# Kernel optimization log

Hardware: AMD Instinct MI355X
Metric: run time of the kernel (lower is better)

Reference implementation:

```python
import jax, jax.numpy as jnp
import numpy as np

EMBED_DIM = 512
NUM_HEADS = 8
HEAD_DIM = EMBED_DIM // NUM_HEADS


def setup_inputs() -> dict:
    key = jax.random.key(0)
    ks = jax.random.split(key, 6)
    B, S, E = 2, 4096, EMBED_DIM
    scale = 1.0 / np.sqrt(E)
    return {
        "rotation_params": jax.random.normal(ks[0], (E, E), jnp.float32) * scale,
        "entangle_params": jax.random.normal(ks[1], (E, E), jnp.float32) * scale,
        "inputs": jax.random.normal(ks[2], (B, S, E), jnp.float32),
        "w_q": jax.random.normal(ks[3], (E, E), jnp.float32) * scale,
        "w_k": jax.random.normal(ks[4], (E, E), jnp.float32) * scale,
        "w_v": jax.random.normal(ks[5], (E, E), jnp.float32) * scale,
    }


def reference(rotation_params, entangle_params, inputs, w_q, w_k, w_v):
    B, S, E = inputs.shape
    H, D = NUM_HEADS, HEAD_DIM
    # torch nn.Linear(x) = x @ W.T ; then extra matmul with rotation/entangle mats
    q = (inputs @ w_q.T) @ rotation_params  # [B,S,E]
    k = (inputs @ w_k.T) @ entangle_params  # [B,S,E]
    v = inputs @ w_v.T                       # [B,S,E]
    # split heads -> [B,H,S,D]
    q = q.reshape(B, S, H, D).transpose(0, 2, 1, 3)
    k = k.reshape(B, S, H, D).transpose(0, 2, 1, 3)
    v = v.reshape(B, S, H, D).transpose(0, 2, 1, 3)
    scores = jnp.einsum("bhqd,bhkd->bhqk", q, k) / jnp.sqrt(jnp.float32(D))
    attn = jax.nn.softmax(scores, axis=-1)  # dropout p=0 (eval) -> identity
    out = jnp.einsum("bhqk,bhkd->bhqd", attn, v)
    return out.transpose(0, 2, 1, 3).reshape(B, S, E)
```

## Files before the change

kernel.cpp:

```cpp
#include <hip/hip_runtime.h>
#include <cstddef>

#define E 512
#define H 8
#define D 64
#define BATCH 2
#define SEQ 4096

typedef __attribute__((ext_vector_type(8))) short bf16x8;
typedef __attribute__((ext_vector_type(4))) float f32x4;
typedef __attribute__((ext_vector_type(16))) float f32x16;
typedef __attribute__((ext_vector_type(4))) unsigned uint4v;

__device__ __forceinline__ ushort f2bf(float f) {
  unsigned u = __builtin_bit_cast(unsigned, f);
  u += 0x7fff + ((u >> 16) & 1);
  return (ushort)(u >> 16);
}
__device__ __forceinline__ float bf2f(ushort h) {
  return __builtin_bit_cast(float, (unsigned)h << 16);
}
__device__ __forceinline__ unsigned pk_bf16(float lo, float hi) {
#if __has_builtin(__builtin_amdgcn_cvt_pk_bf16_f32)
  typedef __attribute__((ext_vector_type(2))) __bf16 bfv2;
  bfv2 r = __builtin_amdgcn_cvt_pk_bf16_f32(lo, hi);
  return __builtin_bit_cast(unsigned, r);
#else
  return (unsigned)f2bf(lo) | ((unsigned)f2bf(hi) << 16);
#endif
}
__device__ __forceinline__ float fexp2(float x) {
#if __has_builtin(__builtin_amdgcn_exp2f)
  return __builtin_amdgcn_exp2f(x);
#else
  return exp2f(x);
#endif
}
__device__ __forceinline__ void permswap32(unsigned& a, unsigned& b) {
  asm("v_permlane32_swap_b32 %0, %1" : "+v"(a), "+v"(b));
}

__device__ __forceinline__ void cvt8_hl(float4 a, float4 b, uint4& hw,
                                        uint4& lw) {
  float v0 = a.x, v1 = a.y, v2 = a.z, v3 = a.w;
  float v4 = b.x, v5 = b.y, v6 = b.z, v7 = b.w;
  ushort h0 = f2bf(v0), h1 = f2bf(v1), h2 = f2bf(v2), h3 = f2bf(v3);
  ushort h4 = f2bf(v4), h5 = f2bf(v5), h6 = f2bf(v6), h7 = f2bf(v7);
  hw.x = (unsigned)h0 | ((unsigned)h1 << 16);
  hw.y = (unsigned)h2 | ((unsigned)h3 << 16);
  hw.z = (unsigned)h4 | ((unsigned)h5 << 16);
  hw.w = (unsigned)h6 | ((unsigned)h7 << 16);
  lw.x = (unsigned)f2bf(v0 - bf2f(h0)) | ((unsigned)f2bf(v1 - bf2f(h1)) << 16);
  lw.y = (unsigned)f2bf(v2 - bf2f(h2)) | ((unsigned)f2bf(v3 - bf2f(h3)) << 16);
  lw.z = (unsigned)f2bf(v4 - bf2f(h4)) | ((unsigned)f2bf(v5 - bf2f(h5)) << 16);
  lw.w = (unsigned)f2bf(v6 - bf2f(h6)) | ((unsigned)f2bf(v7 - bf2f(h7)) << 16);
}

__global__ __launch_bounds__(256) void fold_tiled(
    const float* __restrict__ wq, const float* __restrict__ wk,
    const float* __restrict__ rot, const float* __restrict__ ent,
    const float* __restrict__ wv, ushort* __restrict__ weffbT) {
  const int z = blockIdx.z;
  const int k = blockIdx.x * 256 + threadIdx.x;
  const int n0 = blockIdx.y * 4;
  if (z == 2) {
#pragma unroll
    for (int t = 0; t < 4; ++t)
      weffbT[(size_t)2 * E * E + (size_t)(n0 + t) * E + k] =
          f2bf(wv[(size_t)(n0 + t) * E + k]);
    return;
  }
  const float* w = z ? wk : wq;
  const float* r = z ? ent : rot;
  float acc[4] = {};
  for (int j0 = 0; j0 < E; j0 += 16) {
    float wv_[16];
#pragma unroll
    for (int u = 0; u < 16; ++u) wv_[u] = w[(size_t)(j0 + u) * E + k];
#pragma unroll
    for (int u = 0; u < 16; ++u)
#pragma unroll
      for (int t = 0; t < 4; ++t)
        acc[t] += wv_[u] * r[(size_t)(j0 + u) * E + n0 + t];
  }
#pragma unroll
  for (int t = 0; t < 4; ++t)
    weffbT[(size_t)z * E * E + (size_t)(n0 + t) * E + k] = f2bf(acc[t]);
}

#define LDQ 72
#define LDS_S 136

__global__ __launch_bounds__(512, 4) void qkv_fused(
    const float* __restrict__ xg, const ushort* __restrict__ weffbT,
    ushort* __restrict__ qg, ushort* __restrict__ kg,
    ushort* __restrict__ vtg) {
  __shared__ ushort sm[(128 + 128 + 192) * LDQ];
  ushort* Ah = sm;
  ushort* Al = sm + 128 * LDQ;
  ushort* Bs = sm + 256 * LDQ;
  ushort* vt_lds = Bs;

  const int lin = blockIdx.y * 8 + blockIdx.x;
  const int nl = (lin & 7) * 64 + (lin >> 3);
  const int head = nl & 7;
  const int m0 = (nl >> 3) * 128;

  const int tid = threadIdx.x;
  const int wave = tid >> 6, lane = tid & 63;
  const int l31 = lane & 31, hi = lane >> 5;
  const int wm = wave & 3, wn = wave >> 2;

  const int ar = tid >> 2, ac8 = (tid & 3) * 8;
  const int b1r = tid >> 2;
  const int b2r = 128 + ((tid >> 2) & 63);

  const float* xrow = xg + (size_t)(m0 + ar) * E + ac8;
  const ushort* b1row =
      weffbT + (size_t)(b1r >> 6) * E * E + (size_t)(head * 64 + (b1r & 63)) * E + ac8;
  const ushort* b2row =
      weffbT + (size_t)2 * E * E + (size_t)(head * 64 + (b2r & 63)) * E + ac8;

  f32x16 acc[3];
  acc[0] = 0.f;
  acc[1] = 0.f;
  acc[2] = 0.f;

  const ushort* Ar = Ah + (wm * 32 + l31) * LDQ;
  const ushort* Lr = Al + (wm * 32 + l31) * LDQ;
  const ushort* Br = Bs + (wn * 96 + l31) * LDQ;

  float4 xv0 = *(const float4*)&xrow[0];
  float4 xv1 = *(const float4*)&xrow[4];
  uint4 pb1 = *(const uint4*)&b1row[0];
  uint4 pb2 = (tid < 256) ? *(const uint4*)&b2row[0] : uint4{0, 0, 0, 0};

  for (int k0 = 0; k0 < E; k0 += 32) {
    __syncthreads();
    {
      uint4 hw, lw;
      cvt8_hl(xv0, xv1, hw, lw);
      *(uint4*)&Ah[ar * LDQ + ac8] = hw;
      *(uint4*)&Al[ar * LDQ + ac8] = lw;
    }
    *(uint4*)&Bs[b1r * LDQ + ac8] = pb1;
    if (tid < 256) *(uint4*)&Bs[b2r * LDQ + ac8] = pb2;
    __syncthreads();

    const int kn = (k0 + 32 < E) ? k0 + 32 : 0;
    xv0 = *(const float4*)&xrow[kn];
    xv1 = *(const float4*)&xrow[kn + 4];
    pb1 = *(const uint4*)&b1row[kn];
    if (tid < 256) pb2 = *(const uint4*)&b2row[kn];

#pragma unroll
    for (int ks = 0; ks < 2; ++ks) {
      bf16x8 ah = *(const bf16x8*)&Ar[ks * 16 + hi * 8];
      bf16x8 al = *(const bf16x8*)&Lr[ks * 16 + hi * 8];
#pragma unroll
      for (int t = 0; t < 3; ++t) {
        bf16x8 bf = *(const bf16x8*)&Br[t * 32 * LDQ + ks * 16 + hi * 8];
        acc[t] =
            __builtin_amdgcn_mfma_f32_32x32x16_bf16(ah, bf, acc[t], 0, 0, 0);
        acc[t] =
            __builtin_amdgcn_mfma_f32_32x32x16_bf16(al, bf, acc[t], 0, 0, 0);
      }
    }
  }

  const int b = m0 >> 12;
  const int s_base = m0 & (SEQ - 1);
  const float QSCALE = 0.125f * 1.44269504f;

#pragma unroll
  for (int t = 0; t < 3; ++t) {
    const int n0 = wn * 96 + t * 32;
    const int w = n0 >> 6;
    if (w != 2) {
      ushort* dst = (w == 0) ? qg : kg;
      const float sc = (w == 0) ? QSCALE : 1.0f;
      const int d = (n0 & 63) + l31;
#pragma unroll
      for (int r = 0; r < 16; ++r) {
        float v = acc[t][r] * sc;
        float vo = __shfl_xor(v, 1);
        if (!(lane & 1)) {
          int s = s_base + wm * 32 + (r & 3) + 8 * (r >> 2) + 4 * hi;
          size_t ix = ((size_t)(b * H + head) * SEQ + s) * D + d;
          *(unsigned*)&dst[ix] = pk_bf16(v, vo);
        }
      }
    }
  }

  __syncthreads();
  if (wn == 1) {
#pragma unroll
    for (int t = 1; t < 3; ++t) {
      const int d = (t - 1) * 32 + l31;
#pragma unroll
      for (int g = 0; g < 4; ++g) {
        uint2 w2;
        w2.x = pk_bf16(acc[t][g * 4 + 0], acc[t][g * 4 + 1]);
        w2.y = pk_bf16(acc[t][g * 4 + 2], acc[t][g * 4 + 3]);
        int s = wm * 32 + 8 * g + 4 * hi;
        *(uint2*)&vt_lds[d * LDS_S + s] = w2;
      }
    }
  }
  __syncthreads();
  {
    int vr = tid >> 3, vs = (tid & 7) * 16;
    uint4 c0 = *(const uint4*)&vt_lds[vr * LDS_S + vs];
    uint4 c1 = *(const uint4*)&vt_lds[vr * LDS_S + vs + 8];
    size_t vo = ((size_t)(b * H + head) * D + vr) * SEQ + s_base + vs;
    *(uint4*)&vtg[vo] = c0;
    *(uint4*)&vtg[vo + 8] = c1;
  }
}

#define LDK 72

__global__ __launch_bounds__(512, 4) void attn_mfma(
    const ushort* __restrict__ qg, const ushort* __restrict__ kg,
    const ushort* __restrict__ vtg, float* __restrict__ out) {
  __shared__ ushort sm[4 * 64 * LDK + 256];
  ushort* Ks0 = sm;
  ushort* Vs0 = sm + 2 * 64 * LDK;
  float* lex = (float*)(sm + 4 * 64 * LDK);

  const int qt = blockIdx.x;
  const int bh = blockIdx.y;
  const int tid = threadIdx.x;
  const int wave = tid >> 6;
  const int grp = wave >> 2, wq = wave & 3;
  const int lane = tid & 63;
  const int l31 = lane & 31, hi = lane >> 5;
  const int gtid = tid & 255;

  const ushort* qp = qg + (size_t)bh * SEQ * D;
  const ushort* kp = kg + (size_t)bh * SEQ * D;
  const ushort* vp = vtg + (size_t)bh * D * SEQ;
  ushort* Ksg = Ks0 + grp * 64 * LDK;
  ushort* Vsg = Vs0 + grp * 64 * LDK;

  const int qrow0 = qt * 128 + wq * 32;
  bf16x8 qf[4];
#pragma unroll
  for (int ds = 0; ds < 4; ++ds)
    qf[ds] =
        *(const bf16x8*)&qp[(size_t)(qrow0 + l31) * D + ds * 16 + hi * 8];

  f32x16 o[2];
  o[0] = 0.f;
  o[1] = 0.f;
  float l_r = 0.f;

  const int r0 = gtid >> 3, c0 = (gtid & 7) * 8;
  const int r1 = 32 + r0;

  uint4 pk0 = *(const uint4*)&kp[(size_t)(grp * 64 + r0) * D + c0];
  uint4 pk1 = *(const uint4*)&kp[(size_t)(grp * 64 + r1) * D + c0];
  uint4 pv0 = *(const uint4*)&vp[(size_t)r0 * SEQ + grp * 64 + c0];
  uint4 pv1 = *(const uint4*)&vp[(size_t)r1 * SEQ + grp * 64 + c0];

  for (int it = 0; it < SEQ / 128; ++it) {
    __syncthreads();
    *(uint4*)&Ksg[r0 * LDK + c0] = pk0;
    *(uint4*)&Ksg[r1 * LDK + c0] = pk1;
    *(uint4*)&Vsg[r0 * LDK + c0] = pv0;
    *(uint4*)&Vsg[r1 * LDK + c0] = pv1;
    __syncthreads();

    {
      const int itn = (it + 1 < SEQ / 128) ? it + 1 : it;
      const int ktn = itn * 2 + grp;
      const ushort* ksrc = kp + (size_t)ktn * 64 * D;
      pk0 = *(const uint4*)&ksrc[r0 * D + c0];
      pk1 = *(const uint4*)&ksrc[r1 * D + c0];
      pv0 = *(const uint4*)&vp[(size_t)r0 * SEQ + ktn * 64 + c0];
      pv1 = *(const uint4*)&vp[(size_t)r1 * SEQ + ktn * 64 + c0];
    }

    __builtin_amdgcn_s_setprio(1);
    f32x16 st0 = 0.f, st1 = 0.f;
#pragma unroll
    for (int ds = 0; ds < 4; ++ds) {
      bf16x8 kf0 = *(const bf16x8*)&Ksg[(l31)*LDK + ds * 16 + hi * 8];
      bf16x8 kf1 = *(const bf16x8*)&Ksg[(32 + l31) * LDK + ds * 16 + hi * 8];
      st0 = __builtin_amdgcn_mfma_f32_32x32x16_bf16(kf0, qf[ds], st0, 0, 0, 0);
      st1 = __builtin_amdgcn_mfma_f32_32x32x16_bf16(kf1, qf[ds], st1, 0, 0, 0);
    }

    bf16x8 pf00, pf01;
    {
      float pv[16];
#pragma unroll
      for (int r = 0; r < 16; ++r) pv[r] = fexp2(st0[r]);
      float s01 = (pv[0] + pv[1]) + (pv[2] + pv[3]);
      float s23 = (pv[4] + pv[5]) + (pv[6] + pv[7]);
      float s45 = (pv[8] + pv[9]) + (pv[10] + pv[11]);
      float s67 = (pv[12] + pv[13]) + (pv[14] + pv[15]);
      l_r += (s01 + s23) + (s45 + s67);
      unsigned w0[4], w1[4];
#pragma unroll
      for (int j = 0; j < 2; ++j) {
        {
          unsigned c0w = pk_bf16(pv[2 * j + 0], pv[2 * j + 1]);
          unsigned c1w = pk_bf16(pv[2 * j + 4], pv[2 * j + 5]);
          permswap32(c0w, c1w);
          w0[j] = c0w;
          w0[2 + j] = c1w;
        }
        {
          unsigned c0w = pk_bf16(pv[2 * j + 8], pv[2 * j + 9]);
          unsigned c1w = pk_bf16(pv[2 * j + 12], pv[2 * j + 13]);
          permswap32(c0w, c1w);
          w1[j] = c0w;
          w1[2 + j] = c1w;
        }
      }
      pf00 = __builtin_bit_cast(bf16x8, (uint4v){w0[0], w0[1], w0[2], w0[3]});
      pf01 = __builtin_bit_cast(bf16x8, (uint4v){w1[0], w1[1], w1[2], w1[3]});
    }
#pragma unroll
    for (int nt = 0; nt < 2; ++nt) {
      bf16x8 vf0 = *(const bf16x8*)&Vsg[(nt * 32 + l31) * LDK + hi * 8];
      o[nt] =
          __builtin_amdgcn_mfma_f32_32x32x16_bf16(pf00, vf0, o[nt], 0, 0, 0);
      bf16x8 vf1 = *(const bf16x8*)&Vsg[(nt * 32 + l31) * LDK + 16 + hi * 8];
      o[nt] =
          __builtin_amdgcn_mfma_f32_32x32x16_bf16(pf01, vf1, o[nt], 0, 0, 0);
    }

    bf16x8 pf10, pf11;
    {
      float pv[16];
#pragma unroll
      for (int r = 0; r < 16; ++r) pv[r] = fexp2(st1[r]);
      float s01 = (pv[0] + pv[1]) + (pv[2] + pv[3]);
      float s23 = (pv[4] + pv[5]) + (pv[6] + pv[7]);
      float s45 = (pv[8] + pv[9]) + (pv[10] + pv[11]);
      float s67 = (pv[12] + pv[13]) + (pv[14] + pv[15]);
      l_r += (s01 + s23) + (s45 + s67);
      unsigned w0[4], w1[4];
#pragma unroll
      for (int j = 0; j < 2; ++j) {
        {
          unsigned c0w = pk_bf16(pv[2 * j + 0], pv[2 * j + 1]);
          unsigned c1w = pk_bf16(pv[2 * j + 4], pv[2 * j + 5]);
          permswap32(c0w, c1w);
          w0[j] = c0w;
          w0[2 + j] = c1w;
        }
        {
          unsigned c0w = pk_bf16(pv[2 * j + 8], pv[2 * j + 9]);
          unsigned c1w = pk_bf16(pv[2 * j + 12], pv[2 * j + 13]);
          permswap32(c0w, c1w);
          w1[j] = c0w;
          w1[2 + j] = c1w;
        }
      }
      pf10 = __builtin_bit_cast(bf16x8, (uint4v){w0[0], w0[1], w0[2], w0[3]});
      pf11 = __builtin_bit_cast(bf16x8, (uint4v){w1[0], w1[1], w1[2], w1[3]});
    }
#pragma unroll
    for (int nt = 0; nt < 2; ++nt) {
      bf16x8 vf0 = *(const bf16x8*)&Vsg[(nt * 32 + l31) * LDK + 32 + hi * 8];
      o[nt] =
          __builtin_amdgcn_mfma_f32_32x32x16_bf16(pf10, vf0, o[nt], 0, 0, 0);
      bf16x8 vf1 = *(const bf16x8*)&Vsg[(nt * 32 + l31) * LDK + 48 + hi * 8];
      o[nt] =
          __builtin_amdgcn_mfma_f32_32x32x16_bf16(pf11, vf1, o[nt], 0, 0, 0);
    }
    __builtin_amdgcn_s_setprio(0);
  }

  __syncthreads();
  float lg = l_r + __shfl_xor(l_r, 32);
  float* Oex = (float*)sm;
  if (grp == 1) {
#pragma unroll
    for (int nt = 0; nt < 2; ++nt)
#pragma unroll
      for (int r = 0; r < 16; ++r) {
        int row = (r & 3) + 8 * (r >> 2) + 4 * hi;
        Oex[(wq * 32 + row) * 68 + nt * 32 + l31] = o[nt][r];
      }
    if (lane < 32) lex[wq * 32 + l31] = lg;
  }
  __syncthreads();
  if (grp == 0) {
    float linv = 1.f / (lg + lex[wq * 32 + l31]);
    const int b = bh >> 3, h = bh & 7;
#pragma unroll
    for (int r = 0; r < 16; ++r) {
      int row = (r & 3) + 8 * (r >> 2) + 4 * hi;
      float inv = __shfl(linv, row);
      int srow = qt * 128 + wq * 32 + row;
#pragma unroll
      for (int nt = 0; nt < 2; ++nt) {
        float val = o[nt][r] + Oex[(wq * 32 + row) * 68 + nt * 32 + l31];
        out[((size_t)b * SEQ + srow) * E + h * D + nt * 32 + l31] = val * inv;
      }
    }
  }
}

extern "C" void kernel_launch(void* const* d_in, const int* in_sizes, int n_in,
                              void* d_out, int out_size, void* d_ws,
                              size_t ws_size, hipStream_t stream) {
  const float* rot = (const float*)d_in[0];
  const float* ent = (const float*)d_in[1];
  const float* x = (const float*)d_in[2];
  const float* wq = (const float*)d_in[3];
  const float* wk = (const float*)d_in[4];
  const float* wv = (const float*)d_in[5];
  float* out = (float*)d_out;

  const size_t NX = (size_t)BATCH * SEQ * E;
  ushort* weffbT = (ushort*)d_ws;
  ushort* qg = weffbT + 3 * E * E;
  ushort* kg = qg + NX;
  ushort* vtg = kg + NX;

  fold_tiled<<<dim3(E / 256, E / 4, 3), 256, 0, stream>>>(wq, wk, rot, ent, wv,
                                                          weffbT);
  qkv_fused<<<dim3(H, BATCH * SEQ / 128), 512, 0, stream>>>(x, weffbT, qg, kg,
                                                            vtg);
  attn_mfma<<<dim3(SEQ / 128, BATCH * H), 512, 0, stream>>>(qg, kg, vtg, out);
}
```

Baseline: 226.4 us.

## Split attention key range across four wave groups with 64-row query tiles

The attention kernel now gives each block 64 query rows handled by 2 waves per group, and splits every 128-key chunk across 4 groups of 32 keys instead of 2 groups of 64. The grid doubles and launch bounds request 8 blocks per CU, for more parallelism and better latency hiding. A shared 128-key K/V tile is loaded cooperatively each iteration. The cost is a two-stage cross-group reduction of partial outputs and denominators through LDS with extra barriers, and K/V reloads per block double because each block covers fewer query rows.

```diff
diff --git a/kernel.cpp b/kernel.cpp
--- a/kernel.cpp
+++ b/kernel.cpp
@@ -220,31 +220,28 @@
 }
 
 #define LDK 72
-
-__global__ __launch_bounds__(512, 4) void attn_mfma(
+#define LDV 136
+
+__global__ __launch_bounds__(512, 8) void attn_mfma(
     const ushort* __restrict__ qg, const ushort* __restrict__ kg,
     const ushort* __restrict__ vtg, float* __restrict__ out) {
-  __shared__ ushort sm[4 * 64 * LDK + 256];
-  ushort* Ks0 = sm;
-  ushort* Vs0 = sm + 2 * 64 * LDK;
-  float* lex = (float*)(sm + 4 * 64 * LDK);
+  __shared__ ushort Kall[128 * LDK];
+  __shared__ ushort Vall[64 * LDV];
+  __shared__ float lexA[64], lexB[64];
 
   const int qt = blockIdx.x;
   const int bh = blockIdx.y;
   const int tid = threadIdx.x;
   const int wave = tid >> 6;
-  const int grp = wave >> 2, wq = wave & 3;
+  const int grp = wave >> 1, wq = wave & 1;
   const int lane = tid & 63;
   const int l31 = lane & 31, hi = lane >> 5;
-  const int gtid = tid & 255;
 
   const ushort* qp = qg + (size_t)bh * SEQ * D;
   const ushort* kp = kg + (size_t)bh * SEQ * D;
   const ushort* vp = vtg + (size_t)bh * D * SEQ;
-  ushort* Ksg = Ks0 + grp * 64 * LDK;
-  ushort* Vsg = Vs0 + grp * 64 * LDK;
-
-  const int qrow0 = qt * 128 + wq * 32;
+
+  const int qrow0 = qt * 64 + wq * 32;
   bf16x8 qf[4];
 #pragma unroll
   for (int ds = 0; ds < 4; ++ds)
@@ -256,47 +253,48 @@
   o[1] = 0.f;
   float l_r = 0.f;
 
-  const int r0 = gtid >> 3, c0 = (gtid & 7) * 8;
-  const int r1 = 32 + r0;
-
-  uint4 pk0 = *(const uint4*)&kp[(size_t)(grp * 64 + r0) * D + c0];
-  uint4 pk1 = *(const uint4*)&kp[(size_t)(grp * 64 + r1) * D + c0];
-  uint4 pv0 = *(const uint4*)&vp[(size_t)r0 * SEQ + grp * 64 + c0];
-  uint4 pv1 = *(const uint4*)&vp[(size_t)r1 * SEQ + grp * 64 + c0];
+  const int kr = tid >> 2, kc = (tid & 3) * 16;
+  const int vr = tid >> 3, vc = (tid & 7) * 16;
+
+  uint4 pk0 = *(const uint4*)&kp[(size_t)kr * D + kc];
+  uint4 pk1 = *(const uint4*)&kp[(size_t)kr * D + kc + 8];
+  uint4 pv0 = *(const uint4*)&vp[(size_t)vr * SEQ + vc];
+  uint4 pv1 = *(const uint4*)&vp[(size_t)vr * SEQ + vc + 8];
+
+  const int kb = grp * 32;
 
   for (int it = 0; it < SEQ / 128; ++it) {
     __syncthreads();
-    *(uint4*)&Ksg[r0 * LDK + c0] = pk0;
-    *(uint4*)&Ksg[r1 * LDK + c0] = pk1;
-    *(uint4*)&Vsg[r0 * LDK + c0] = pv0;
-    *(uint4*)&Vsg[r1 * LDK + c0] = pv1;
+    *(uint4*)&Kall[kr * LDK + kc] = pk0;
+    *(uint4*)&Kall[kr * LDK + kc + 8] = pk1;
+    *(uint4*)&Vall[vr * LDV + vc] = pv0;
+    *(uint4*)&Vall[vr * LDV + vc + 8] = pv1;
     __syncthreads();
 
     {
       const int itn = (it + 1 < SEQ / 128) ? it + 1 : it;
-      const int ktn = itn * 2 + grp;
-      const ushort* ksrc = kp + (size_t)ktn * 64 * D;
-      pk0 = *(const uint4*)&ksrc[r0 * D + c0];
-      pk1 = *(const uint4*)&ksrc[r1 * D + c0];
-      pv0 = *(const uint4*)&vp[(size_t)r0 * SEQ + ktn * 64 + c0];
-      pv1 = *(const uint4*)&vp[(size_t)r1 * SEQ + ktn * 64 + c0];
+      const int base = itn * 128;
+      pk0 = *(const uint4*)&kp[(size_t)(base + kr) * D + kc];
+      pk1 = *(const uint4*)&kp[(size_t)(base + kr) * D + kc + 8];
+      pv0 = *(const uint4*)&vp[(size_t)vr * SEQ + base + vc];
+      pv1 = *(const uint4*)&vp[(size_t)vr * SEQ + base + vc + 8];
     }
 
     __builtin_amdgcn_s_setprio(1);
-    f32x16 st0 = 0.f, st1 = 0.f;
+    f32x16 st = 0.f;
 #pragma unroll
     for (int ds = 0; ds < 4; ++ds) {
-      bf16x8 kf0 = *(const bf16x8*)&Ksg[(l31)*LDK + ds * 16 + hi * 8];
-      bf16x8 kf1 = *(const bf16x8*)&Ksg[(32 + l31) * LDK + ds * 16 + hi * 8];
-      st0 = __builtin_amdgcn_mfma_f32_32x32x16_bf16(kf0, qf[ds], st0, 0, 0, 0);
-      st1 = __builtin_amdgcn_mfma_f32_32x32x16_bf16(kf1, qf[ds], st1, 0, 0, 0);
-    }
-
-    bf16x8 pf00, pf01;
+      bf16x8 kf =
+          *(const bf16x8*)&Kall[(kb + l31) * LDK + ds * 16 + hi * 8];
+      st = __builtin_amdgcn_mfma_f32_32x32x16_bf16(kf, qf[ds], st, 0, 0, 0);
+    }
+    __builtin_amdgcn_s_setprio(0);
+
+    bf16x8 pf0, pf1;
     {
       float pv[16];
 #pragma unroll
-      for (int r = 0; r < 16; ++r) pv[r] = fexp2(st0[r]);
+      for (int r = 0; r < 16; ++r) pv[r] = fexp2(st[r]);
       float s01 = (pv[0] + pv[1]) + (pv[2] + pv[3]);
       float s23 = (pv[4] + pv[5]) + (pv[6] + pv[7]);
       float s45 = (pv[8] + pv[9]) + (pv[10] + pv[11]);
@@ -320,87 +318,92 @@
           w1[2 + j] = c1w;
         }
       }
-      pf00 = __builtin_bit_cast(bf16x8, (uint4v){w0[0], w0[1], w0[2], w0[3]});
-      pf01 = __builtin_bit_cast(bf16x8, (uint4v){w1[0], w1[1], w1[2], w1[3]});
-    }
+      pf0 = __builtin_bit_cast(bf16x8, (uint4v){w0[0], w0[1], w0[2], w0[3]});
+      pf1 = __builtin_bit_cast(bf16x8, (uint4v){w1[0], w1[1], w1[2], w1[3]});
+    }
+
+    __builtin_amdgcn_s_setprio(1);
 #pragma unroll
     for (int nt = 0; nt < 2; ++nt) {
-      bf16x8 vf0 = *(const bf16x8*)&Vsg[(nt * 32 + l31) * LDK + hi * 8];
-      o[nt] =
-          __builtin_amdgcn_mfma_f32_32x32x16_bf16(pf00, vf0, o[nt], 0, 0, 0);
-      bf16x8 vf1 = *(const bf16x8*)&Vsg[(nt * 32 + l31) * LDK + 16 + hi * 8];
-      o[nt] =
-          __builtin_amdgcn_mfma_f32_32x32x16_bf16(pf01, vf1, o[nt], 0, 0, 0);
-    }
-
-    bf16x8 pf10, pf11;
-    {
-      float pv[16];
-#pragma unroll
-      for (int r = 0; r < 16; ++r) pv[r] = fexp2(st1[r]);
-      float s01 = (pv[0] + pv[1]) + (pv[2] + pv[3]);
-      float s23 = (pv[4] + pv[5]) + (pv[6] + pv[7]);
-      float s45 = (pv[8] + pv[9]) + (pv[10] + pv[11]);
-      float s67 = (pv[12] + pv[13]) + (pv[14] + pv[15]);
-      l_r += (s01 + s23) + (s45 + s67);
-      unsigned w0[4], w1[4];
-#pragma unroll
-      for (int j = 0; j < 2; ++j) {
-        {
-          unsigned c0w = pk_bf16(pv[2 * j + 0], pv[2 * j + 1]);
-          unsigned c1w = pk_bf16(pv[2 * j + 4], pv[2 * j + 5]);
-          permswap32(c0w, c1w);
-          w0[j] = c0w;
-          w0[2 + j] = c1w;
-        }
-        {
-          unsigned c0w = pk_bf16(pv[2 * j + 8], pv[2 * j + 9]);
-          unsigned c1w = pk_bf16(pv[2 * j + 12], pv[2 * j + 13]);
-          permswap32(c0w, c1w);
-          w1[j] = c0w;
-          w1[2 + j] = c1w;
-        }
-      }
-      pf10 = __builtin_bit_cast(bf16x8, (uint4v){w0[0], w0[1], w0[2], w0[3]});
-      pf11 = __builtin_bit_cast(bf16x8, (uint4v){w1[0], w1[1], w1[2], w1[3]});
-    }
-#pragma unroll
-    for (int nt = 0; nt < 2; ++nt) {
-      bf16x8 vf0 = *(const bf16x8*)&Vsg[(nt * 32 + l31) * LDK + 32 + hi * 8];
-      o[nt] =
-          __builtin_amdgcn_mfma_f32_32x32x16_bf16(pf10, vf0, o[nt], 0, 0, 0);
-      bf16x8 vf1 = *(const bf16x8*)&Vsg[(nt * 32 + l31) * LDK + 48 + hi * 8];
-      o[nt] =
-          __builtin_amdgcn_mfma_f32_32x32x16_bf16(pf11, vf1, o[nt], 0, 0, 0);
+      bf16x8 vf0 =
+          *(const bf16x8*)&Vall[(nt * 32 + l31) * LDV + kb + hi * 8];
+      o[nt] = __builtin_amdgcn_mfma_f32_32x32x16_bf16(pf0, vf0, o[nt], 0, 0, 0);
+      bf16x8 vf1 =
+          *(const bf16x8*)&Vall[(nt * 32 + l31) * LDV + kb + 16 + hi * 8];
+      o[nt] = __builtin_amdgcn_mfma_f32_32x32x16_bf16(pf1, vf1, o[nt], 0, 0, 0);
     }
     __builtin_amdgcn_s_setprio(0);
   }
 
   __syncthreads();
   float lg = l_r + __shfl_xor(l_r, 32);
-  float* Oex = (float*)sm;
+  float* OexA = (float*)Kall;
+  float* OexB = (float*)Vall;
   if (grp == 1) {
 #pragma unroll
     for (int nt = 0; nt < 2; ++nt)
 #pragma unroll
       for (int r = 0; r < 16; ++r) {
         int row = (r & 3) + 8 * (r >> 2) + 4 * hi;
-        Oex[(wq * 32 + row) * 68 + nt * 32 + l31] = o[nt][r];
-      }
-    if (lane < 32) lex[wq * 32 + l31] = lg;
+        OexA[(wq * 32 + row) * 68 + nt * 32 + l31] = o[nt][r];
+      }
+    if (lane < 32) lexA[wq * 32 + l31] = lg;
+  }
+  if (grp == 3) {
+#pragma unroll
+    for (int nt = 0; nt < 2; ++nt)
+#pragma unroll
+      for (int r = 0; r < 16; ++r) {
+        int row = (r & 3) + 8 * (r >> 2) + 4 * hi;
+        OexB[(wq * 32 + row) * 68 + nt * 32 + l31] = o[nt][r];
+      }
+    if (lane < 32) lexB[wq * 32 + l31] = lg;
   }
   __syncthreads();
   if (grp == 0) {
-    float linv = 1.f / (lg + lex[wq * 32 + l31]);
+#pragma unroll
+    for (int nt = 0; nt < 2; ++nt)
+#pragma unroll
+      for (int r = 0; r < 16; ++r) {
+        int row = (r & 3) + 8 * (r >> 2) + 4 * hi;
+        o[nt][r] += OexA[(wq * 32 + row) * 68 + nt * 32 + l31];
+      }
+    lg += lexA[wq * 32 + l31];
+  }
+  if (grp == 2) {
+#pragma unroll
+    for (int nt = 0; nt < 2; ++nt)
+#pragma unroll
+      for (int r = 0; r < 16; ++r) {
+        int row = (r & 3) + 8 * (r >> 2) + 4 * hi;
+        o[nt][r] += OexB[(wq * 32 + row) * 68 + nt * 32 + l31];
+      }
+    lg += lexB[wq * 32 + l31];
+  }
+  __syncthreads();
+  if (grp == 2) {
+#pragma unroll
+    for (int nt = 0; nt < 2; ++nt)
+#pragma unroll
+      for (int r = 0; r < 16; ++r) {
+        int row = (r & 3) + 8 * (r >> 2) + 4 * hi;
+        OexA[(wq * 32 + row) * 68 + nt * 32 + l31] = o[nt][r];
+      }
+    if (lane < 32) lexA[wq * 32 + l31] = lg;
+  }
+  __syncthreads();
+  if (grp == 0) {
+    lg += lexA[wq * 32 + l31];
+    float linv = 1.f / lg;
     const int b = bh >> 3, h = bh & 7;
 #pragma unroll
     for (int r = 0; r < 16; ++r) {
       int row = (r & 3) + 8 * (r >> 2) + 4 * hi;
       float inv = __shfl(linv, row);
-      int srow = qt * 128 + wq * 32 + row;
+      int srow = qt * 64 + wq * 32 + row;
 #pragma unroll
       for (int nt = 0; nt < 2; ++nt) {
-        float val = o[nt][r] + Oex[(wq * 32 + row) * 68 + nt * 32 + l31];
+        float val = o[nt][r] + OexA[(wq * 32 + row) * 68 + nt * 32 + l31];
         out[((size_t)b * SEQ + srow) * E + h * D + nt * 32 + l31] = val * inv;
       }
     }
@@ -428,5 +431,5 @@
                                                           weffbT);
   qkv_fused<<<dim3(H, BATCH * SEQ / 128), 512, 0, stream>>>(x, weffbT, qg, kg,
                                                             vtg);
-  attn_mfma<<<dim3(SEQ / 128, BATCH * H), 512, 0, stream>>>(qg, kg, vtg, out);
-}
+  attn_mfma<<<dim3(SEQ / 64, BATCH * H), 512, 0, stream>>>(qg, kg, vtg, out);
+}
```

Result: slower. 658.3 us (+190.8%).
